# Kernel tuning notes

Measured on AMD Instinct MI355X. Metric: run time of the kernel, lower is better.

Reference implementation:

```python
import jax, jax.numpy as jnp
import numpy as np

DIM0, DIMO, WIDTH, DEPTH = 64, 16, 128, 6  # depth = number of weight matrices
N = 524288


def setup_inputs() -> dict:
    key = jax.random.key(0)
    ks = jax.random.split(key, DEPTH + 1)
    x = jax.random.normal(ks[0], (N, DIM0), dtype=jnp.float32)
    bd0 = 1.0 / np.sqrt(DIM0)   # first layer init bound (per torch code)
    bd = 1.0 / np.sqrt(WIDTH)   # remaining layers init bound
    W0 = jax.random.uniform(ks[1], (DIM0, WIDTH), minval=-bd0, maxval=bd0, dtype=jnp.float32)
    W1 = jax.random.uniform(ks[2], (WIDTH, WIDTH), minval=-bd, maxval=bd, dtype=jnp.float32)
    W2 = jax.random.uniform(ks[3], (WIDTH, WIDTH), minval=-bd, maxval=bd, dtype=jnp.float32)
    W3 = jax.random.uniform(ks[4], (WIDTH, WIDTH), minval=-bd, maxval=bd, dtype=jnp.float32)
    W4 = jax.random.uniform(ks[5], (WIDTH, WIDTH), minval=-bd, maxval=bd, dtype=jnp.float32)
    W5 = jax.random.uniform(ks[6], (WIDTH, DIMO), minval=-bd, maxval=bd, dtype=jnp.float32)
    bias = jnp.zeros((DIMO,), dtype=jnp.float32)
    return {"x": x, "W0": W0, "W1": W1, "W2": W2, "W3": W3, "W4": W4, "W5": W5, "bias": bias}


def reference(x, W0, W1, W2, W3, W4, W5, bias):
    # Fully-fused MLP math: matmul (no bias) + ReLU for every layer except the
    # last (output_activation='None'); then cast back to x dtype and add bias.
    h = jax.nn.relu(x @ W0)
    h = jax.nn.relu(h @ W1)
    h = jax.nn.relu(h @ W2)
    h = jax.nn.relu(h @ W3)
    h = jax.nn.relu(h @ W4)
    out = (h @ W5).astype(x.dtype) + bias
    return out
```

## Files before the change

kernel.cpp:

```cpp
#include <hip/hip_runtime.h>
#include <stdint.h>


typedef __bf16 bf16x8 __attribute__((ext_vector_type(8)));
typedef float  floatx4 __attribute__((ext_vector_type(4)));

#define GAS __attribute__((address_space(1)))
#define LAS __attribute__((address_space(3)))

constexpr int NS   = 524288;
constexpr int SPW  = 64;
constexpr int NBLK = NS / (8 * SPW);

constexpr int WTOT = 9472;

__device__ __host__ __forceinline__ int kappa(int s) {
  return 32 * (s >> 5) + 16 * ((s >> 2) & 1) + 4 * ((s >> 3) & 3) + (s & 3);
}

__global__ void prep_weights(const float* __restrict__ W0, const float* __restrict__ W1,
                             const float* __restrict__ W2, const float* __restrict__ W3,
                             const float* __restrict__ W4, const float* __restrict__ W5,
                             bf16x8* __restrict__ ws) {
  int gid = blockIdx.x * blockDim.x + threadIdx.x;
  if (gid >= WTOT) return;
  const float* Wsrc; int nout, kt_n, base, ident;
  if (gid < 1024)      { Wsrc = W0; nout = 128; kt_n = 2; base = 0;    ident = 1; }
  else if (gid < 3072) { Wsrc = W1; nout = 128; kt_n = 4; base = 1024; ident = 0; }
  else if (gid < 5120) { Wsrc = W2; nout = 128; kt_n = 4; base = 3072; ident = 0; }
  else if (gid < 7168) { Wsrc = W3; nout = 128; kt_n = 4; base = 5120; ident = 0; }
  else if (gid < 9216) { Wsrc = W4; nout = 128; kt_n = 4; base = 7168; ident = 0; }
  else                 { Wsrc = W5; nout = 16;  kt_n = 4; base = 9216; ident = 0; }
  int id   = gid - base;
  int lane = id & 63;
  int frag = id >> 6;
  int kt   = frag % kt_n;
  int rb   = frag / kt_n;
  int outf = rb * 16 + (lane & 15);
  int gg   = lane >> 4;
  bf16x8 v;
#pragma unroll
  for (int e = 0; e < 8; ++e) {
    int s  = 32 * kt + 8 * gg + e;
    int in = ident ? s : kappa(s);
    v[e] = (__bf16)Wsrc[in * nout + outf];
  }
  ws[gid] = v;
}

__device__ __forceinline__ void zero_acc(floatx4 acc[8][4]) {
  floatx4 z = {0.f, 0.f, 0.f, 0.f};
#pragma unroll
  for (int ot = 0; ot < 8; ++ot)
#pragma unroll
    for (int i = 0; i < 4; ++i) acc[ot][i] = z;
}

__device__ __forceinline__ void pack_relu(const floatx4 acc[8][4], bf16x8 B[4][4]) {
#pragma unroll
  for (int kt = 0; kt < 4; ++kt)
#pragma unroll
    for (int i = 0; i < 4; ++i) {
      floatx4 u = acc[2 * kt][i], v = acc[2 * kt + 1][i];
      bf16x8 b;
      b[0] = (__bf16)fmaxf(u[0], 0.f); b[1] = (__bf16)fmaxf(u[1], 0.f);
      b[2] = (__bf16)fmaxf(u[2], 0.f); b[3] = (__bf16)fmaxf(u[3], 0.f);
      b[4] = (__bf16)fmaxf(v[0], 0.f); b[5] = (__bf16)fmaxf(v[1], 0.f);
      b[6] = (__bf16)fmaxf(v[2], 0.f); b[7] = (__bf16)fmaxf(v[3], 0.f);
      B[kt][i] = b;
    }
}

__global__ void __launch_bounds__(512, 2) mlp_kernel(const float* __restrict__ x,
                                                     const float* __restrict__ bias,
                                                     const bf16x8* __restrict__ wimg,
                                                     float* __restrict__ out) {
  __shared__ bf16x8 Wlds[WTOT];

  const int t    = threadIdx.x;
  const int lane = t & 63;
  const int l15  = lane & 15;
  const int g    = lane >> 4;
  const int w    = __builtin_amdgcn_readfirstlane(t >> 6);

#pragma unroll
  for (int r = 0; r < 19; ++r) {
    int base = r * 512 + w * 64;
    if (base < WTOT)
      __builtin_amdgcn_global_load_lds((const GAS void*)(wimg + base + lane),
                                       (LAS void*)(Wlds + base), 16, 0, 0);
  }
  __syncthreads();

  const int wid = __builtin_amdgcn_readfirstlane(blockIdx.x * 8 + w);
  const size_t sbase = (size_t)wid * SPW;

  bf16x8  B[4][4];
  floatx4 acc[8][4];

  const float* xw = x + sbase * 64;
#pragma unroll
  for (int kt = 0; kt < 2; ++kt)
#pragma unroll
    for (int i = 0; i < 4; ++i) {
      const floatx4* p = (const floatx4*)(xw + (16 * i + l15) * 64 + 32 * kt + 8 * g);
      floatx4 lo = p[0], hi = p[1];
      bf16x8 v;
      v[0] = (__bf16)lo[0]; v[1] = (__bf16)lo[1]; v[2] = (__bf16)lo[2]; v[3] = (__bf16)lo[3];
      v[4] = (__bf16)hi[0]; v[5] = (__bf16)hi[1]; v[6] = (__bf16)hi[2]; v[7] = (__bf16)hi[3];
      B[kt][i] = v;
    }

  zero_acc(acc);
#pragma unroll
  for (int kt = 0; kt < 2; ++kt) {
    bf16x8 a[8];
#pragma unroll
    for (int ot = 0; ot < 8; ++ot)
      a[ot] = Wlds[(ot * 2 + kt) * 64 + lane];
#pragma unroll
    for (int ot = 0; ot < 8; ++ot)
#pragma unroll
      for (int i = 0; i < 4; ++i)
        acc[ot][i] = __builtin_amdgcn_mfma_f32_16x16x32_bf16(a[ot], B[kt][i], acc[ot][i], 0, 0, 0);
    __builtin_amdgcn_sched_barrier(0);
  }

  constexpr int WOFFH[4] = {1024, 3072, 5120, 7168};
#pragma unroll
  for (int l = 0; l < 4; ++l) {
    pack_relu(acc, B);
    zero_acc(acc);
    const bf16x8* Wl = Wlds + WOFFH[l];
#pragma unroll
    for (int kt = 0; kt < 4; ++kt) {
      bf16x8 a[8];
#pragma unroll
      for (int ot = 0; ot < 8; ++ot)
        a[ot] = Wl[(ot * 4 + kt) * 64 + lane];
#pragma unroll
      for (int ot = 0; ot < 8; ++ot)
#pragma unroll
        for (int i = 0; i < 4; ++i)
          acc[ot][i] = __builtin_amdgcn_mfma_f32_16x16x32_bf16(a[ot], B[kt][i], acc[ot][i], 0, 0, 0);
      __builtin_amdgcn_sched_barrier(0);
    }
  }

  pack_relu(acc, B);
  floatx4 o[4];
  {
    floatx4 z = {0.f, 0.f, 0.f, 0.f};
    o[0] = z; o[1] = z; o[2] = z; o[3] = z;
  }
#pragma unroll
  for (int kt = 0; kt < 4; ++kt) {
    bf16x8 a = Wlds[9216 + kt * 64 + lane];
#pragma unroll
    for (int i = 0; i < 4; ++i)
      o[i] = __builtin_amdgcn_mfma_f32_16x16x32_bf16(a, B[kt][i], o[i], 0, 0, 0);
  }
  floatx4 bv = *(const floatx4*)(bias + 4 * g);
  floatx4* outv = (floatx4*)out;
#pragma unroll
  for (int i = 0; i < 4; ++i) {
    size_t s = sbase + 16 * i + l15;
    outv[s * 4 + g] = o[i] + bv;
  }
}

extern "C" void kernel_launch(void* const* d_in, const int* in_sizes, int n_in,
                              void* d_out, int out_size, void* d_ws, size_t ws_size,
                              hipStream_t stream) {
  (void)in_sizes; (void)n_in; (void)out_size; (void)ws_size;
  const float* x    = (const float*)d_in[0];
  const float* W0   = (const float*)d_in[1];
  const float* W1   = (const float*)d_in[2];
  const float* W2   = (const float*)d_in[3];
  const float* W3   = (const float*)d_in[4];
  const float* W4   = (const float*)d_in[5];
  const float* W5   = (const float*)d_in[6];
  const float* bias = (const float*)d_in[7];
  bf16x8* ws = (bf16x8*)d_ws;

  prep_weights<<<(WTOT + 255) / 256, 256, 0, stream>>>(W0, W1, W2, W3, W4, W5, ws);
  mlp_kernel<<<NBLK, 512, 0, stream>>>(x, bias, (const bf16x8*)ws, (float*)d_out);
}
```

Before: 254.1 us.

## Double-buffer LDS weight fragments across MFMA half-tiles and drop accumulator zeroing

Restructures each layer into half-output-tile steps and keeps two register buffers of weight fragments, so the LDS reads for the next step are issued before the MFMAs of the current step. The next layer's first fragments are prefetched during the last step of the current layer. Accumulator zeroing is replaced by passing a zero operand to the first MFMA of each layer. This aims to hide LDS read latency behind matrix work, at some cost in register pressure under the 2-block occupancy bound.

```diff
diff --git a/kernel.cpp b/kernel.cpp
--- a/kernel.cpp
+++ b/kernel.cpp
@@ -48,14 +48,6 @@
   ws[gid] = v;
 }
 
-__device__ __forceinline__ void zero_acc(floatx4 acc[8][4]) {
-  floatx4 z = {0.f, 0.f, 0.f, 0.f};
-#pragma unroll
-  for (int ot = 0; ot < 8; ++ot)
-#pragma unroll
-    for (int i = 0; i < 4; ++i) acc[ot][i] = z;
-}
-
 __device__ __forceinline__ void pack_relu(const floatx4 acc[8][4], bf16x8 B[4][4]) {
 #pragma unroll
   for (int kt = 0; kt < 4; ++kt)
@@ -70,6 +62,38 @@
       B[kt][i] = b;
     }
 }
+
+#define SB __builtin_amdgcn_sched_barrier(0)
+#define LDH(buf, fb, fs) do {                      \
+    buf[0] = Wlds[(fb) * 64 + lane];               \
+    buf[1] = Wlds[((fb) + (fs)) * 64 + lane];      \
+    buf[2] = Wlds[((fb) + 2 * (fs)) * 64 + lane];  \
+    buf[3] = Wlds[((fb) + 3 * (fs)) * 64 + lane];  \
+  } while (0)
+#define MMZ(buf, kt, oh) do {                                                             \
+    _Pragma("unroll") for (int j = 0; j < 4; ++j) {                                       \
+      _Pragma("unroll") for (int i = 0; i < 4; ++i)                                       \
+        acc[(oh) * 4 + j][i] =                                                            \
+            __builtin_amdgcn_mfma_f32_16x16x32_bf16(buf[j], B[kt][i], z, 0, 0, 0);        \
+    }                                                                                     \
+  } while (0)
+#define MMA(buf, kt, oh) do {                                                             \
+    _Pragma("unroll") for (int j = 0; j < 4; ++j) {                                       \
+      _Pragma("unroll") for (int i = 0; i < 4; ++i)                                       \
+        acc[(oh) * 4 + j][i] = __builtin_amdgcn_mfma_f32_16x16x32_bf16(                   \
+            buf[j], B[kt][i], acc[(oh) * 4 + j][i], 0, 0, 0);                             \
+    }                                                                                     \
+  } while (0)
+#define HLAYER(Fb, NB, NS_) do {                   \
+    LDH(A1, (Fb) + 16, 4); MMZ(A0, 0, 0); SB;      \
+    LDH(A0, (Fb) + 1,  4); MMZ(A1, 0, 1); SB;      \
+    LDH(A1, (Fb) + 17, 4); MMA(A0, 1, 0); SB;      \
+    LDH(A0, (Fb) + 2,  4); MMA(A1, 1, 1); SB;      \
+    LDH(A1, (Fb) + 18, 4); MMA(A0, 2, 0); SB;      \
+    LDH(A0, (Fb) + 3,  4); MMA(A1, 2, 1); SB;      \
+    LDH(A1, (Fb) + 19, 4); MMA(A0, 3, 0); SB;      \
+    LDH(A0, (NB), (NS_)); MMA(A1, 3, 1); SB;       \
+  } while (0)
 
 __global__ void __launch_bounds__(512, 2) mlp_kernel(const float* __restrict__ x,
                                                      const float* __restrict__ bias,
@@ -97,6 +121,10 @@
 
   bf16x8  B[4][4];
   floatx4 acc[8][4];
+  bf16x8  A0[4], A1[4];
+  floatx4 z = {0.f, 0.f, 0.f, 0.f};
+
+  LDH(A0, 0, 2);
 
   const float* xw = x + sbase * 64;
 #pragma unroll
@@ -111,55 +139,27 @@
       B[kt][i] = v;
     }
 
-  zero_acc(acc);
+  LDH(A1, 8, 2);  MMZ(A0, 0, 0); SB;
+  LDH(A0, 1, 2);  MMZ(A1, 0, 1); SB;
+  LDH(A1, 9, 2);  MMA(A0, 1, 0); SB;
+  LDH(A0, 16, 4); MMA(A1, 1, 1); SB;
+  pack_relu(acc, B);
+
+  HLAYER(16,  48, 4);  pack_relu(acc, B);
+  HLAYER(48,  80, 4);  pack_relu(acc, B);
+  HLAYER(80, 112, 4);  pack_relu(acc, B);
+  HLAYER(112, 144, 1); pack_relu(acc, B);
+
+  floatx4 o[4];
 #pragma unroll
-  for (int kt = 0; kt < 2; ++kt) {
-    bf16x8 a[8];
+  for (int i = 0; i < 4; ++i)
+    o[i] = __builtin_amdgcn_mfma_f32_16x16x32_bf16(A0[0], B[0][i], z, 0, 0, 0);
 #pragma unroll
-    for (int ot = 0; ot < 8; ++ot)
-      a[ot] = Wlds[(ot * 2 + kt) * 64 + lane];
-#pragma unroll
-    for (int ot = 0; ot < 8; ++ot)
-#pragma unroll
-      for (int i = 0; i < 4; ++i)
-        acc[ot][i] = __builtin_amdgcn_mfma_f32_16x16x32_bf16(a[ot], B[kt][i], acc[ot][i], 0, 0, 0);
-    __builtin_amdgcn_sched_barrier(0);
-  }
-
-  constexpr int WOFFH[4] = {1024, 3072, 5120, 7168};
-#pragma unroll
-  for (int l = 0; l < 4; ++l) {
-    pack_relu(acc, B);
-    zero_acc(acc);
-    const bf16x8* Wl = Wlds + WOFFH[l];
-#pragma unroll
-    for (int kt = 0; kt < 4; ++kt) {
-      bf16x8 a[8];
-#pragma unroll
-      for (int ot = 0; ot < 8; ++ot)
-        a[ot] = Wl[(ot * 4 + kt) * 64 + lane];
-#pragma unroll
-      for (int ot = 0; ot < 8; ++ot)
-#pragma unroll
-        for (int i = 0; i < 4; ++i)
-          acc[ot][i] = __builtin_amdgcn_mfma_f32_16x16x32_bf16(a[ot], B[kt][i], acc[ot][i], 0, 0, 0);
-      __builtin_amdgcn_sched_barrier(0);
-    }
-  }
-
-  pack_relu(acc, B);
-  floatx4 o[4];
-  {
-    floatx4 z = {0.f, 0.f, 0.f, 0.f};
-    o[0] = z; o[1] = z; o[2] = z; o[3] = z;
-  }
-#pragma unroll
-  for (int kt = 0; kt < 4; ++kt) {
-    bf16x8 a = Wlds[9216 + kt * 64 + lane];
+  for (int kt = 1; kt < 4; ++kt)
 #pragma unroll
     for (int i = 0; i < 4; ++i)
-      o[i] = __builtin_amdgcn_mfma_f32_16x16x32_bf16(a, B[kt][i], o[i], 0, 0, 0);
-  }
+      o[i] = __builtin_amdgcn_mfma_f32_16x16x32_bf16(A0[kt], B[kt][i], o[i], 0, 0, 0);
+
   floatx4 bv = *(const floatx4*)(bias + 4 * g);
   floatx4* outv = (floatx4*)out;
 #pragma unroll
```

Result: slower. 261.7 us (+3.0%).
